# Performance work log

Hardware: AMD Instinct MI355X
Metric: run time of the kernel (lower is better)

Reference implementation:

```python
import jax, jax.numpy as jnp
from jax import lax
import numpy as np

B, T, F, H, L = 256, 512, 16, 256, 2


def _lstm_layer(x, w_ih, w_hh, b_ih, b_hh):
    # x: [B, T, in]; w_ih: [4H, in]; w_hh: [4H, H]; biases: [4H]
    # PyTorch gate order: i, f, g, o
    x_proj = jnp.einsum('bti,gi->btg', x, w_ih) + b_ih + b_hh  # [B, T, 4H]
    h0 = jnp.zeros((x.shape[0], w_hh.shape[1]), x.dtype)
    c0 = h0

    def step(carry, xp):
        h, c = carry
        gates = xp + h @ w_hh.T  # [B, 4H]
        i, f, g, o = jnp.split(gates, 4, axis=-1)
        c = jax.nn.sigmoid(f) * c + jax.nn.sigmoid(i) * jnp.tanh(g)
        h = jax.nn.sigmoid(o) * jnp.tanh(c)
        return (h, c), h

    _, hs = lax.scan(step, (h0, c0), jnp.swapaxes(x_proj, 0, 1))  # [T, B, H]
    return jnp.swapaxes(hs, 0, 1)  # [B, T, H]


def setup_inputs() -> dict:
    key = jax.random.key(0)
    ks = jax.random.split(key, 16)
    x = jax.random.normal(ks[0], (B, T, F), dtype=jnp.float32)
    lengths = jax.random.randint(ks[1], (B,), 1, T + 1)  # in [1, T]
    s = 1.0 / np.sqrt(H)
    u = lambda k, shape: jax.random.uniform(k, shape, jnp.float32, -s, s)
    inp = {'x': x, 'lengths': lengths}
    in_dims = [F, H]
    for l in range(L):
        inp[f'w_ih{l}'] = u(ks[2 + 4 * l], (4 * H, in_dims[l]))
        inp[f'w_hh{l}'] = u(ks[3 + 4 * l], (4 * H, H))
        inp[f'b_ih{l}'] = u(ks[4 + 4 * l], (4 * H,))
        inp[f'b_hh{l}'] = u(ks[5 + 4 * l], (4 * H,))
    inp['fc_w'] = u(ks[10], (1, H))
    inp['fc_b'] = u(ks[11], (1,))
    return inp


def reference(x, lengths, w_ih0, w_hh0, b_ih0, b_hh0,
              w_ih1, w_hh1, b_ih1, b_hh1, fc_w, fc_b):
    # Packed LSTM: outputs at t >= length never influence last_outputs
    # (recurrence only flows forward in time), so running the dense
    # full-length LSTM and gathering at lengths-1 is mathematically identical.
    h = _lstm_layer(x, w_ih0, w_hh0, b_ih0, b_hh0)
    h = _lstm_layer(h, w_ih1, w_hh1, b_ih1, b_hh1)
    last = h[jnp.arange(h.shape[0]), lengths - 1]  # [B, H]
    return jax.nn.relu(last) @ fc_w.T + fc_b  # [B, 1]
```

## Files before the change

kernel.cpp:

```cpp
#include <hip/hip_runtime.h>
#include <hip/hip_fp16.h>


#define Tc 32
#define NCHUNK 16

#define OFF_IH0   0
#define OFF_B0    16384
#define OFF_B1    17408
#define OFF_C0S   18432
#define OFF_C1S   84480
#define OFF_H1S   150528
#define OFF_HLAST 216576
#define FP_END    282624
#define H_HH0  0
#define H_HH1  262144
#define H_IH1  524288
#define H_H0C  786432
#define H0SLOT 2113536
#define H_XP1  5013504
#define XPSLOT 8454144

#define SMEM_BYTES 85184

typedef _Float16 v2h __attribute__((ext_vector_type(2)));

__device__ __forceinline__ unsigned packh2(float a, float b) {
  __half2 h = __floats2half2_rn(a, b);
  return *(unsigned*)&h;
}
__device__ __forceinline__ float4 dot4(const float4 w, const v2h h, float4 acc) {
  const v2h* wg = (const v2h*)&w;
  acc.x = __builtin_amdgcn_fdot2(wg[0], h, acc.x, false);
  acc.y = __builtin_amdgcn_fdot2(wg[1], h, acc.y, false);
  acc.z = __builtin_amdgcn_fdot2(wg[2], h, acc.z, false);
  acc.w = __builtin_amdgcn_fdot2(wg[3], h, acc.w, false);
  return acc;
}
__device__ __forceinline__ float sigf(float x) {
  return __fdividef(1.f, 1.f + __expf(-x));
}
__device__ __forceinline__ float tanhf_fast(float x) {
  float ax = fabsf(x);
  float e = __expf(-2.f * ax);
  float t = __fdividef(1.f - e, 1.f + e);
  return copysignf(t, x);
}
__device__ __forceinline__ float h2f(unsigned short s) {
  __half h = __builtin_bit_cast(__half, s);
  return __half2float(h);
}
__device__ __forceinline__ float4 cvt4(ushort4 v) {
  float4 r;
  r.x = h2f(v.x); r.y = h2f(v.y); r.z = h2f(v.z); r.w = h2f(v.w);
  return r;
}
__device__ __forceinline__ v2h u2h(unsigned v) {
  return __builtin_bit_cast(v2h, v);
}
__device__ __forceinline__ float4 f4add(float4 a, float4 b) {
  a.x += b.x; a.y += b.y; a.z += b.z; a.w += b.w;
  return a;
}

__global__ __launch_bounds__(256) void prep_kernel(
    const float* __restrict__ w_ih0, const float* __restrict__ w_hh0,
    const float* __restrict__ b_ih0, const float* __restrict__ b_hh0,
    const float* __restrict__ w_ih1, const float* __restrict__ w_hh1,
    const float* __restrict__ b_ih1, const float* __restrict__ b_hh1,
    float* __restrict__ ws) {
  const int idx = blockIdx.x * blockDim.x + threadIdx.x;
  const int g = idx & 3, u = (idx >> 2) & 255, p = idx >> 10;
  const int j = g * 256 + u;
  unsigned* h16u = (unsigned*)(ws + FP_END);
  h16u[H_HH0 / 2 + idx] = packh2(w_hh0[j * 256 + 2 * p], w_hh0[j * 256 + 2 * p + 1]);
  h16u[H_HH1 / 2 + idx] = packh2(w_hh1[j * 256 + 2 * p], w_hh1[j * 256 + 2 * p + 1]);
  h16u[H_IH1 / 2 + idx] = packh2(w_ih1[j * 256 + 2 * p], w_ih1[j * 256 + 2 * p + 1]);
  if (idx < 8192) {
    ((unsigned*)(ws + OFF_IH0))[idx] =
        packh2(w_ih0[j * 16 + 2 * p], w_ih0[j * 16 + 2 * p + 1]);
  }
  if (idx < 1024) {
    ws[OFF_B0 + idx] = b_ih0[j] + b_hh0[j];
    ws[OFF_B1 + idx] = b_ih1[j] + b_hh1[j];
  }
}

__global__ __launch_bounds__(1024) void fused_kernel(
    float* __restrict__ ws, const float* __restrict__ x,
    const int* __restrict__ lengths, int step) {
  extern __shared__ __align__(16) char smem_raw[];
  const int bid = blockIdx.x;
  const int tid = threadIdx.x;
  __half* h16 = (__half*)(ws + FP_END);
  unsigned short* h0cS = (unsigned short*)(h16 + H_H0C);
  unsigned short* xpS = (unsigned short*)(h16 + H_XP1);

  if (bid < 86) {
    if (step >= NCHUNK) return;
    const int kc = step;
    const int kq = tid >> 8, u = tid & 255;
    const int bg = bid * 3;
    unsigned short* hb = (unsigned short*)smem_raw;
    unsigned* xsp = (unsigned*)(smem_raw + 3072);
    float4* sc4 = (float4*)(smem_raw + 3264);
    float4* wxl = (float4*)(smem_raw + 52416);

    int len[3];
    #pragma unroll
    for (int b = 0; b < 3; ++b) len[b] = (bg + b < 256) ? lengths[bg + b] : 1;
    const int tmaxb = max(len[0], max(len[1], len[2]));
    if (kc * Tc >= tmaxb) return;
    const int tend = min(Tc, tmaxb - kc * Tc);
    const int slot = kc & 1, slotP = slot ^ 1;

    {
      const float4* gwx = (const float4*)(ws + OFF_IH0);
      wxl[tid] = gwx[tid];
      wxl[tid + 1024] = gwx[tid + 1024];
    }

    const float4* wq = (const float4*)(h16 + H_HH0) + (size_t)(kq * 32) * 256 + u;
    const float4 bias = ((const float4*)(ws + OFF_B0))[u];

    float cc = 0.f;
    if (kq < 3) {
      unsigned short hv = 0;
      if (kc > 0) {
        hv = h0cS[(size_t)slotP * H0SLOT + ((size_t)(bg + kq) * 32 + 31) * 256 + u];
        cc = ws[OFF_C0S + (bg + kq) * 256 + u];
      }
      hb[0 * 768 + kq * 256 + u] = hv;
    }
    if (tid < 24) {
      int b = tid >> 3, i = tid & 7;
      int bb = min(bg + b, 255);
      const float* xp = x + (size_t)bb * 8192 + (kc * Tc) * 16;
      xsp[0 * 24 + b * 8 + i] = packh2(xp[2 * i], xp[2 * i + 1]);
    }
    __syncthreads();

    for (int tc = 0; tc < tend; ++tc) {
      const int cur = tc & 1, nxt = cur ^ 1;
      float4 A0, A1, A2;
      if (kq == 3) {
        A0 = bias; A1 = bias; A2 = bias;
        #pragma unroll
        for (int p = 0; p < 8; ++p) {
          float4 w = wxl[p * 256 + u];
          A0 = dot4(w, u2h(xsp[cur * 24 + 0 * 8 + p]), A0);
          A1 = dot4(w, u2h(xsp[cur * 24 + 1 * 8 + p]), A1);
          A2 = dot4(w, u2h(xsp[cur * 24 + 2 * 8 + p]), A2);
        }
      } else {
        A0 = make_float4(0, 0, 0, 0); A1 = A0; A2 = A0;
      }

      {
        const float4* h0r0 = (const float4*)(hb + cur * 768 + 0 * 256 + kq * 64);
        const float4* h0r1 = (const float4*)(hb + cur * 768 + 1 * 256 + kq * 64);
        const float4* h0r2 = (const float4*)(hb + cur * 768 + 2 * 256 + kq * 64);
        float4 B[3][4];
        #pragma unroll
        for (int p = 0; p < 4; ++p) {
          B[0][p] = wq[p * 256];
          B[1][p] = wq[(4 + p) * 256];
        }
        #pragma unroll
        for (int g = 0; g < 8; ++g) {
          if (g + 2 < 8) {
            #pragma unroll
            for (int p = 0; p < 4; ++p)
              B[(g + 2) % 3][p] = wq[((g + 2) * 4 + p) * 256];
          }
          const float4* wbuf = B[g % 3];
          float4 h40 = h0r0[g], h41 = h0r1[g], h42 = h0r2[g];
          const v2h* hp0 = (const v2h*)&h40;
          const v2h* hp1 = (const v2h*)&h41;
          const v2h* hp2 = (const v2h*)&h42;
          #pragma unroll
          for (int q = 0; q < 4; ++q) {
            A0 = dot4(wbuf[q], hp0[q], A0);
            A1 = dot4(wbuf[q], hp1[q], A1);
            A2 = dot4(wbuf[q], hp2[q], A2);
          }
        }
      }

      sc4[(kq * 3 + 0) * 256 + u] = A0;
      sc4[(kq * 3 + 1) * 256 + u] = A1;
      sc4[(kq * 3 + 2) * 256 + u] = A2;
      __syncthreads();

      if (kq < 3) {
        float4 A = f4add(f4add(sc4[(0 * 3 + kq) * 256 + u],
                               sc4[(1 * 3 + kq) * 256 + u]),
                         f4add(sc4[(2 * 3 + kq) * 256 + u],
                               sc4[(3 * 3 + kq) * 256 + u]));
        float ig = sigf(A.x), fg = sigf(A.y);
        float gg = tanhf_fast(A.z), og = sigf(A.w);
        cc = fg * cc + ig * gg;
        float h = og * tanhf_fast(cc);
        unsigned short hu = __half_as_ushort(__float2half(h));
        hb[nxt * 768 + kq * 256 + u] = hu;
        h0cS[(size_t)slot * H0SLOT + ((size_t)(bg + kq) * 32 + tc) * 256 + u] = hu;
      } else if (tid >= 768 && tid < 792) {
        int bi = tid - 768, b = bi >> 3, i = bi & 7;
        int bb = min(bg + b, 255);
        int tn = min(kc * Tc + tc + 1, 511);
        const float* xp = x + (size_t)bb * 8192 + tn * 16;
        xsp[nxt * 24 + b * 8 + i] = packh2(xp[2 * i], xp[2 * i + 1]);
      }
      __syncthreads();
    }
    if (kq < 3) ws[OFF_C0S + (bg + kq) * 256 + u] = cc;

  } else if (bid < 172) {
    if (step < 2 || step >= NCHUNK + 2) return;
    const int kc = step - 2;
    const int kq = tid >> 8, u = tid & 255;
    const int bg = (bid - 86) * 3;
    unsigned short* h1b = (unsigned short*)smem_raw;
    float4* sc4 = (float4*)(smem_raw + 3072);

    int len[3];
    #pragma unroll
    for (int b = 0; b < 3; ++b) len[b] = (bg + b < 256) ? lengths[bg + b] : 1;
    const int tmaxb = max(len[0], max(len[1], len[2]));
    if (kc * Tc >= tmaxb) return;
    const int tend = min(Tc, tmaxb - kc * Tc);
    const int slot = kc & 1;

    const float4* wq = (const float4*)(h16 + H_HH1) + (size_t)(kq * 32) * 256 + u;

    float cc = 0.f, hout = 0.f;
    int lenb = 1;
    const unsigned short* xb = xpS;
    ushort4 xc;
    if (kq < 3) {
      lenb = len[kq];
      float hv = 0.f;
      if (kc > 0) {
        hv = ws[OFF_H1S + (bg + kq) * 256 + u];
        cc = ws[OFF_C1S + (bg + kq) * 256 + u];
      }
      h1b[0 * 768 + kq * 256 + u] = __half_as_ushort(__float2half(hv));
      xb = xpS + (size_t)slot * XPSLOT + (size_t)(bg + kq) * 32768 + u * 4;
      xc = *(const ushort4*)(xb);
    }
    __syncthreads();

    for (int tc = 0; tc < tend; ++tc) {
      const int cur = tc & 1, nxt = cur ^ 1;
      float4 A0 = make_float4(0, 0, 0, 0), A1 = A0, A2 = A0;

      {
        const float4* r0 = (const float4*)(h1b + cur * 768 + 0 * 256 + kq * 64);
        const float4* r1 = (const float4*)(h1b + cur * 768 + 1 * 256 + kq * 64);
        const float4* r2 = (const float4*)(h1b + cur * 768 + 2 * 256 + kq * 64);
        float4 B[3][4];
        #pragma unroll
        for (int p = 0; p < 4; ++p) {
          B[0][p] = wq[p * 256];
          B[1][p] = wq[(4 + p) * 256];
        }
        #pragma unroll
        for (int g = 0; g < 8; ++g) {
          if (g + 2 < 8) {
            #pragma unroll
            for (int p = 0; p < 4; ++p)
              B[(g + 2) % 3][p] = wq[((g + 2) * 4 + p) * 256];
          }
          const float4* wbuf = B[g % 3];
          float4 h40 = r0[g], h41 = r1[g], h42 = r2[g];
          const v2h* hp0 = (const v2h*)&h40;
          const v2h* hp1 = (const v2h*)&h41;
          const v2h* hp2 = (const v2h*)&h42;
          #pragma unroll
          for (int q = 0; q < 4; ++q) {
            A0 = dot4(wbuf[q], hp0[q], A0);
            A1 = dot4(wbuf[q], hp1[q], A1);
            A2 = dot4(wbuf[q], hp2[q], A2);
          }
        }
      }

      sc4[(kq * 3 + 0) * 256 + u] = A0;
      sc4[(kq * 3 + 1) * 256 + u] = A1;
      sc4[(kq * 3 + 2) * 256 + u] = A2;
      __syncthreads();

      if (kq < 3) {
        ushort4 xn;
        if (tc + 1 < tend) xn = *(const ushort4*)(xb + (tc + 1) * 1024);
        float4 A = f4add(f4add(sc4[(0 * 3 + kq) * 256 + u],
                               sc4[(1 * 3 + kq) * 256 + u]),
                         f4add(sc4[(2 * 3 + kq) * 256 + u],
                               sc4[(3 * 3 + kq) * 256 + u]));
        A = f4add(A, cvt4(xc));
        float ig = sigf(A.x), fg = sigf(A.y);
        float gg = tanhf_fast(A.z), og = sigf(A.w);
        cc = fg * cc + ig * gg;
        float h = og * tanhf_fast(cc);
        hout = h;
        h1b[nxt * 768 + kq * 256 + u] = __half_as_ushort(__float2half(h));
        const int t = kc * Tc + tc;
        if (t == lenb - 1) ws[OFF_HLAST + (bg + kq) * 256 + u] = h;
        xc = xn;
      }
      __syncthreads();
    }
    if (kq < 3) {
      ws[OFF_C1S + (bg + kq) * 256 + u] = cc;
      ws[OFF_H1S + (bg + kq) * 256 + u] = hout;
    }

  } else {
    if (step < 1 || step >= NCHUNK + 1) return;
    if (bid >= 236) return;
    const int kc = step - 1;
    const int gid = bid - 172;
    const int b0g = gid * 4;
    const int rp = tid >> 9;
    const int rt = tid & 63, wv = (tid >> 6) & 7;
    __half2* hc2 = (__half2*)smem_raw;

    int lmax = 0;
    #pragma unroll
    for (int i = 0; i < 4; ++i) lmax = max(lmax, lengths[b0g + i]);
    if (kc * Tc >= lmax) return;
    const int slot = kc & 1;

    {
      const unsigned short* src =
          h0cS + (size_t)slot * H0SLOT + (size_t)b0g * 8192;
      const int cl = tid & 127, pg = tid >> 7;
      #pragma unroll
      for (int pp = 0; pp < 16; pp += 4) {
        const int p0 = pg * 16 + pp;
        uint4 v = *(const uint4*)(src + (size_t)cl * 256 + p0 * 2);
        unsigned* d = (unsigned*)hc2;
        d[(p0 + 0) * 128 + cl] = v.x;
        d[(p0 + 1) * 128 + cl] = v.y;
        d[(p0 + 2) * 128 + cl] = v.z;
        d[(p0 + 3) * 128 + cl] = v.w;
      }
    }
    __syncthreads();

    const __half* Wb = h16 + H_IH1;
    unsigned short* xdst = xpS + (size_t)slot * XPSLOT;
    #pragma unroll 1
    for (int cp = 0; cp < 2; ++cp) {
      const int uA = rp * 128 + rt, uB = uA + 64;
      const int c0 = cp * 64 + wv * 8;
      const float4 bA = ((const float4*)(ws + OFF_B1))[uA];
      const float4 bB = ((const float4*)(ws + OFF_B1))[uB];
      float accA[4][8], accB[4][8];
      #pragma unroll
      for (int g = 0; g < 4; ++g)
        #pragma unroll
        for (int cc = 0; cc < 8; ++cc) {
          accA[g][cc] = ((const float*)&bA)[g];
          accB[g][cc] = ((const float*)&bB)[g];
        }
      #pragma unroll 2
      for (int p = 0; p < 128; ++p) {
        float4 wA = *(const float4*)(Wb + (size_t)p * 2048 + uA * 8);
        float4 wB = *(const float4*)(Wb + (size_t)p * 2048 + uB * 8);
        float4 h0v = *(const float4*)(hc2 + p * 128 + c0);
        float4 h1v = *(const float4*)(hc2 + p * 128 + c0 + 4);
        const v2h* ga = (const v2h*)&wA;
        const v2h* gb = (const v2h*)&wB;
        const v2h* hv = (const v2h*)&h0v;
        const v2h* hw = (const v2h*)&h1v;
        #pragma unroll
        for (int g = 0; g < 4; ++g) {
          #pragma unroll
          for (int cc = 0; cc < 4; ++cc) {
            accA[g][cc] = __builtin_amdgcn_fdot2(ga[g], hv[cc], accA[g][cc], false);
            accA[g][cc + 4] = __builtin_amdgcn_fdot2(ga[g], hw[cc], accA[g][cc + 4], false);
            accB[g][cc] = __builtin_amdgcn_fdot2(gb[g], hv[cc], accB[g][cc], false);
            accB[g][cc + 4] = __builtin_amdgcn_fdot2(gb[g], hw[cc], accB[g][cc + 4], false);
          }
        }
      }
      #pragma unroll
      for (int cc = 0; cc < 8; ++cc) {
        const int col = c0 + cc;
        const size_t cb = ((size_t)(b0g + (col >> 5)) * 32 + (col & 31)) * 1024;
        ushort4 oA, oB;
        oA.x = __half_as_ushort(__float2half(accA[0][cc]));
        oA.y = __half_as_ushort(__float2half(accA[1][cc]));
        oA.z = __half_as_ushort(__float2half(accA[2][cc]));
        oA.w = __half_as_ushort(__float2half(accA[3][cc]));
        oB.x = __half_as_ushort(__float2half(accB[0][cc]));
        oB.y = __half_as_ushort(__float2half(accB[1][cc]));
        oB.z = __half_as_ushort(__float2half(accB[2][cc]));
        oB.w = __half_as_ushort(__float2half(accB[3][cc]));
        *(ushort4*)(xdst + cb + uA * 4) = oA;
        *(ushort4*)(xdst + cb + uB * 4) = oB;
      }
    }
  }
}

__global__ __launch_bounds__(256) void fc_kernel(
    const float* __restrict__ ws, const float* __restrict__ fc_w,
    const float* __restrict__ fc_b, float* __restrict__ out) {
  __shared__ float red[256];
  const int tid = threadIdx.x;
  const int b = blockIdx.x;
  red[tid] = fmaxf(ws[OFF_HLAST + b * 256 + tid], 0.f) * fc_w[tid];
  __syncthreads();
  #pragma unroll
  for (int s = 128; s > 0; s >>= 1) {
    if (tid < s) red[tid] += red[tid + s];
    __syncthreads();
  }
  if (tid == 0) out[b] = red[0] + fc_b[0];
}

extern "C" void kernel_launch(void* const* d_in, const int* in_sizes, int n_in,
                              void* d_out, int out_size, void* d_ws, size_t ws_size,
                              hipStream_t stream) {
  const float* x     = (const float*)d_in[0];
  const int*   lens  = (const int*)d_in[1];
  const float* w_ih0 = (const float*)d_in[2];
  const float* w_hh0 = (const float*)d_in[3];
  const float* b_ih0 = (const float*)d_in[4];
  const float* b_hh0 = (const float*)d_in[5];
  const float* w_ih1 = (const float*)d_in[6];
  const float* w_hh1 = (const float*)d_in[7];
  const float* b_ih1 = (const float*)d_in[8];
  const float* b_hh1 = (const float*)d_in[9];
  const float* fc_w  = (const float*)d_in[10];
  const float* fc_b  = (const float*)d_in[11];
  float* out = (float*)d_out;
  float* ws  = (float*)d_ws;

  hipLaunchKernelGGL(prep_kernel, dim3(512), dim3(256), 0, stream,
                     w_ih0, w_hh0, b_ih0, b_hh0, w_ih1, w_hh1, b_ih1, b_hh1, ws);
  hipFuncSetAttribute(reinterpret_cast<const void*>(fused_kernel),
                      hipFuncAttributeMaxDynamicSharedMemorySize, SMEM_BYTES);
  for (int k = 0; k < NCHUNK + 2; ++k) {
    hipLaunchKernelGGL(fused_kernel, dim3(236), dim3(1024), SMEM_BYTES, stream,
                       ws, x, lens, k);
  }
  hipLaunchKernelGGL(fc_kernel, dim3(256), dim3(256), 0, stream,
                     ws, fc_w, fc_b, out);
}
```

Before: 3.338 ms.

## Use MFMA 16x16x32 for LSTM recurrences with 16-sequence blocks

Replaces the fdot2-based recurrent matvec, which processed 3 sequences per block with a cross-wave shared-memory reduction, by MFMA f16 16x16x32 tiles. Each block now handles 16 batch rows, and each wave owns 16 hidden units across all 4 gates. Weights are repacked into MFMA fragment layout, and the layer-1 input projection output is re-laid out to match the accumulator fragments. This drops the per-step partial-sum reduction and its extra barrier, and cuts the recurrent blocks from 172 to 32. In exchange, much less of the GPU is occupied during the serial recurrence, and per-block serial length grows with the longest sequence in each group of 16.

```diff
diff --git a/kernel.cpp b/kernel.cpp
--- a/kernel.cpp
+++ b/kernel.cpp
@@ -21,21 +21,14 @@
 #define H_XP1  5013504
 #define XPSLOT 8454144
 
-#define SMEM_BYTES 85184
-
-typedef _Float16 v2h __attribute__((ext_vector_type(2)));
+#define SMEM_BYTES 32768
+
+typedef _Float16 v8h __attribute__((ext_vector_type(8)));
+typedef float v4f __attribute__((ext_vector_type(4)));
 
 __device__ __forceinline__ unsigned packh2(float a, float b) {
   __half2 h = __floats2half2_rn(a, b);
   return *(unsigned*)&h;
-}
-__device__ __forceinline__ float4 dot4(const float4 w, const v2h h, float4 acc) {
-  const v2h* wg = (const v2h*)&w;
-  acc.x = __builtin_amdgcn_fdot2(wg[0], h, acc.x, false);
-  acc.y = __builtin_amdgcn_fdot2(wg[1], h, acc.y, false);
-  acc.z = __builtin_amdgcn_fdot2(wg[2], h, acc.z, false);
-  acc.w = __builtin_amdgcn_fdot2(wg[3], h, acc.w, false);
-  return acc;
 }
 __device__ __forceinline__ float sigf(float x) {
   return __fdividef(1.f, 1.f + __expf(-x));
@@ -50,18 +43,13 @@
   __half h = __builtin_bit_cast(__half, s);
   return __half2float(h);
 }
-__device__ __forceinline__ float4 cvt4(ushort4 v) {
-  float4 r;
-  r.x = h2f(v.x); r.y = h2f(v.y); r.z = h2f(v.z); r.w = h2f(v.w);
-  return r;
-}
-__device__ __forceinline__ v2h u2h(unsigned v) {
-  return __builtin_bit_cast(v2h, v);
-}
-__device__ __forceinline__ float4 f4add(float4 a, float4 b) {
-  a.x += b.x; a.y += b.y; a.z += b.z; a.w += b.w;
-  return a;
-}
+__device__ __forceinline__ float h_at(uint4 v, int i) {
+  unsigned wd = ((const unsigned*)&v)[i >> 1];
+  unsigned short s = (i & 1) ? (unsigned short)(wd >> 16) : (unsigned short)wd;
+  return h2f(s);
+}
+
+typedef _Float16 v2h __attribute__((ext_vector_type(2)));
 
 __global__ __launch_bounds__(256) void prep_kernel(
     const float* __restrict__ w_ih0, const float* __restrict__ w_hh0,
@@ -70,17 +58,35 @@
     const float* __restrict__ b_ih1, const float* __restrict__ b_hh1,
     float* __restrict__ ws) {
   const int idx = blockIdx.x * blockDim.x + threadIdx.x;
-  const int g = idx & 3, u = (idx >> 2) & 255, p = idx >> 10;
-  const int j = g * 256 + u;
   unsigned* h16u = (unsigned*)(ws + FP_END);
-  h16u[H_HH0 / 2 + idx] = packh2(w_hh0[j * 256 + 2 * p], w_hh0[j * 256 + 2 * p + 1]);
-  h16u[H_HH1 / 2 + idx] = packh2(w_hh1[j * 256 + 2 * p], w_hh1[j * 256 + 2 * p + 1]);
-  h16u[H_IH1 / 2 + idx] = packh2(w_ih1[j * 256 + 2 * p], w_ih1[j * 256 + 2 * p + 1]);
-  if (idx < 8192) {
-    ((unsigned*)(ws + OFF_IH0))[idx] =
-        packh2(w_ih0[j * 16 + 2 * p], w_ih0[j * 16 + 2 * p + 1]);
+  {
+    const int q2 = idx * 2;
+    const int j = q2 & 7, l = (q2 >> 3) & 63, ks = (q2 >> 9) & 7;
+    const int U = (q2 >> 12) & 15, g = q2 >> 16;
+    const int row = g * 256 + U * 16 + (l & 15);
+    const int k0 = ks * 32 + ((l >> 4) & 3) * 8 + j;
+    h16u[H_HH0 / 2 + idx] =
+        packh2(w_hh0[row * 256 + k0], w_hh0[row * 256 + k0 + 1]);
+    h16u[H_HH1 / 2 + idx] =
+        packh2(w_hh1[row * 256 + k0], w_hh1[row * 256 + k0 + 1]);
+  }
+  {
+    const int g = idx & 3, u = (idx >> 2) & 255, p = idx >> 10;
+    const int j = g * 256 + u;
+    h16u[H_IH1 / 2 + idx] =
+        packh2(w_ih1[j * 256 + 2 * p], w_ih1[j * 256 + 2 * p + 1]);
+  }
+  if (idx < 16384) {
+    const int q2 = idx * 2;
+    const int j = q2 & 7, l = (q2 >> 3) & 63, U = (q2 >> 9) & 15, g = q2 >> 13;
+    const int row = g * 256 + U * 16 + (l & 15);
+    const int k0 = (l >> 4) * 8 + j;
+    float a = (k0 < 16) ? w_ih0[row * 16 + k0] : 0.f;
+    float b = (k0 + 1 < 16) ? w_ih0[row * 16 + k0 + 1] : 0.f;
+    ((unsigned*)(ws + OFF_IH0))[idx] = packh2(a, b);
   }
   if (idx < 1024) {
+    const int j = (idx & 3) * 256 + (idx >> 2);
     ws[OFF_B0 + idx] = b_ih0[j] + b_hh0[j];
     ws[OFF_B1 + idx] = b_ih1[j] + b_hh1[j];
   }
@@ -96,311 +102,262 @@
   unsigned short* h0cS = (unsigned short*)(h16 + H_H0C);
   unsigned short* xpS = (unsigned short*)(h16 + H_XP1);
 
-  if (bid < 86) {
-    if (step >= NCHUNK) return;
-    const int kc = step;
-    const int kq = tid >> 8, u = tid & 255;
-    const int bg = bid * 3;
-    unsigned short* hb = (unsigned short*)smem_raw;
-    unsigned* xsp = (unsigned*)(smem_raw + 3072);
-    float4* sc4 = (float4*)(smem_raw + 3264);
-    float4* wxl = (float4*)(smem_raw + 52416);
-
-    int len[3];
-    #pragma unroll
-    for (int b = 0; b < 3; ++b) len[b] = (bg + b < 256) ? lengths[bg + b] : 1;
-    const int tmaxb = max(len[0], max(len[1], len[2]));
+  if (bid < 32) {
+    const bool isL0 = (bid < 16);
+    int kc;
+    if (isL0) { if (step >= NCHUNK) return; kc = step; }
+    else { if (step < 2 || step >= NCHUNK + 2) return; kc = step - 2; }
+    const int G = isL0 ? bid : (bid - 16);
+    const int bg = G * 16;
+    const int w = tid >> 6, l = tid & 63;
+    const int n = l & 15, m0 = (l >> 4) * 4;
+    const int u = w * 16 + n;
+    unsigned short* hf = (unsigned short*)smem_raw;
+    unsigned short* xf = hf + 8192;
+
+    int tmaxb = 1;
+    for (int i = 0; i < 16; ++i) tmaxb = max(tmaxb, lengths[bg + i]);
     if (kc * Tc >= tmaxb) return;
     const int tend = min(Tc, tmaxb - kc * Tc);
     const int slot = kc & 1, slotP = slot ^ 1;
 
-    {
-      const float4* gwx = (const float4*)(ws + OFF_IH0);
-      wxl[tid] = gwx[tid];
-      wxl[tid + 1024] = gwx[tid + 1024];
-    }
-
-    const float4* wq = (const float4*)(h16 + H_HH0) + (size_t)(kq * 32) * 256 + u;
-    const float4 bias = ((const float4*)(ws + OFF_B0))[u];
-
-    float cc = 0.f;
-    if (kq < 3) {
+    const float4* WB =
+        (const float4*)(h16 + (isL0 ? H_HH0 : H_HH1));
+    const int ksp = u >> 5, lp0 = ((u >> 3) & 3) * 16, jh = u & 7;
+
+    float bias[4];
+    v8h bx[4];
+    if (isL0) {
+      const float4* WX = (const float4*)(ws + OFF_IH0);
+      #pragma unroll
+      for (int g = 0; g < 4; ++g) {
+        bx[g] = __builtin_bit_cast(v8h, WX[(g * 16 + w) * 64 + l]);
+        bias[g] = ws[OFF_B0 + u * 4 + g];
+      }
+    }
+    int len4[4];
+    #pragma unroll
+    for (int r = 0; r < 4; ++r) len4[r] = lengths[bg + m0 + r];
+
+    float c4[4] = {0.f, 0.f, 0.f, 0.f};
+    float h4[4] = {0.f, 0.f, 0.f, 0.f};
+    #pragma unroll
+    for (int r = 0; r < 4; ++r) {
       unsigned short hv = 0;
       if (kc > 0) {
-        hv = h0cS[(size_t)slotP * H0SLOT + ((size_t)(bg + kq) * 32 + 31) * 256 + u];
-        cc = ws[OFF_C0S + (bg + kq) * 256 + u];
-      }
-      hb[0 * 768 + kq * 256 + u] = hv;
-    }
-    if (tid < 24) {
-      int b = tid >> 3, i = tid & 7;
-      int bb = min(bg + b, 255);
-      const float* xp = x + (size_t)bb * 8192 + (kc * Tc) * 16;
-      xsp[0 * 24 + b * 8 + i] = packh2(xp[2 * i], xp[2 * i + 1]);
-    }
+        if (isL0) {
+          hv = h0cS[(size_t)slotP * H0SLOT +
+                    ((size_t)(bg + m0 + r) * 32 + 31) * 256 + u];
+          c4[r] = ws[OFF_C0S + (bg + m0 + r) * 256 + u];
+        } else {
+          hv = __half_as_ushort(
+              __float2half(ws[OFF_H1S + (bg + m0 + r) * 256 + u]));
+          c4[r] = ws[OFF_C1S + (bg + m0 + r) * 256 + u];
+        }
+      }
+      hf[(ksp * 64 + lp0 + m0 + r) * 8 + jh] = hv;
+    }
+    const unsigned short* xpb = nullptr;
+    uint4 q0, q1;
+    if (isL0) {
+      if (w == 0) {
+        if (l >= 32) {
+          uint4 z = {0, 0, 0, 0};
+          *(uint4*)(xf + l * 8) = z;
+          *(uint4*)(xf + (64 + l) * 8) = z;
+        } else {
+          const float* xp =
+              x + (size_t)(bg + (l & 15)) * 8192 + (kc * Tc) * 16 + (l >> 4) * 8;
+          float4 a = *(const float4*)xp, b = *(const float4*)(xp + 4);
+          uint4 v = {packh2(a.x, a.y), packh2(a.z, a.w), packh2(b.x, b.y),
+                     packh2(b.z, b.w)};
+          *(uint4*)(xf + l * 8) = v;
+        }
+      }
+    } else {
+      xpb = xpS + (size_t)slot * XPSLOT + (size_t)G * 524288 + u * 64 + m0 * 4;
+      q0 = *(const uint4*)(xpb);
+      q1 = *(const uint4*)(xpb + 8);
+    }
+    v8h bf[4], bn[4];
+    #pragma unroll
+    for (int g = 0; g < 4; ++g)
+      bf[g] = __builtin_bit_cast(v8h, WB[((g * 16 + w) * 8 + 0) * 64 + l]);
     __syncthreads();
 
     for (int tc = 0; tc < tend; ++tc) {
       const int cur = tc & 1, nxt = cur ^ 1;
-      float4 A0, A1, A2;
-      if (kq == 3) {
-        A0 = bias; A1 = bias; A2 = bias;
-        #pragma unroll
-        for (int p = 0; p < 8; ++p) {
-          float4 w = wxl[p * 256 + u];
-          A0 = dot4(w, u2h(xsp[cur * 24 + 0 * 8 + p]), A0);
-          A1 = dot4(w, u2h(xsp[cur * 24 + 1 * 8 + p]), A1);
-          A2 = dot4(w, u2h(xsp[cur * 24 + 2 * 8 + p]), A2);
-        }
+      v4f A[4];
+      uint4 p0n, p1n;
+      if (isL0) {
+        #pragma unroll
+        for (int g = 0; g < 4; ++g) {
+          v4f bz = {bias[g], bias[g], bias[g], bias[g]};
+          A[g] = bz;
+        }
+        v8h ax = __builtin_bit_cast(v8h, *(const float4*)(xf + (cur * 64 + l) * 8));
+        #pragma unroll
+        for (int g = 0; g < 4; ++g)
+          A[g] = __builtin_amdgcn_mfma_f32_16x16x32_f16(ax, bx[g], A[g], 0, 0, 0);
       } else {
-        A0 = make_float4(0, 0, 0, 0); A1 = A0; A2 = A0;
-      }
-
-      {
-        const float4* h0r0 = (const float4*)(hb + cur * 768 + 0 * 256 + kq * 64);
-        const float4* h0r1 = (const float4*)(hb + cur * 768 + 1 * 256 + kq * 64);
-        const float4* h0r2 = (const float4*)(hb + cur * 768 + 2 * 256 + kq * 64);
-        float4 B[3][4];
-        #pragma unroll
-        for (int p = 0; p < 4; ++p) {
-          B[0][p] = wq[p * 256];
-          B[1][p] = wq[(4 + p) * 256];
-        }
-        #pragma unroll
-        for (int g = 0; g < 8; ++g) {
-          if (g + 2 < 8) {
-            #pragma unroll
-            for (int p = 0; p < 4; ++p)
-              B[(g + 2) % 3][p] = wq[((g + 2) * 4 + p) * 256];
-          }
-          const float4* wbuf = B[g % 3];
-          float4 h40 = h0r0[g], h41 = h0r1[g], h42 = h0r2[g];
-          const v2h* hp0 = (const v2h*)&h40;
-          const v2h* hp1 = (const v2h*)&h41;
-          const v2h* hp2 = (const v2h*)&h42;
+        if (tc + 1 < tend) {
+          p0n = *(const uint4*)(xpb + (size_t)(tc + 1) * 16384);
+          p1n = *(const uint4*)(xpb + (size_t)(tc + 1) * 16384 + 8);
+        }
+        #pragma unroll
+        for (int g = 0; g < 4; ++g) {
+          v4f av;
+          av[0] = h_at(q0, g);
+          av[1] = h_at(q0, 4 + g);
+          av[2] = h_at(q1, g);
+          av[3] = h_at(q1, 4 + g);
+          A[g] = av;
+        }
+      }
+      #pragma unroll
+      for (int ks = 0; ks < 8; ++ks) {
+        if (ks < 7) {
           #pragma unroll
-          for (int q = 0; q < 4; ++q) {
-            A0 = dot4(wbuf[q], hp0[q], A0);
-            A1 = dot4(wbuf[q], hp1[q], A1);
-            A2 = dot4(wbuf[q], hp2[q], A2);
-          }
-        }
-      }
-
-      sc4[(kq * 3 + 0) * 256 + u] = A0;
-      sc4[(kq * 3 + 1) * 256 + u] = A1;
-      sc4[(kq * 3 + 2) * 256 + u] = A2;
+          for (int g = 0; g < 4; ++g)
+            bn[g] = __builtin_bit_cast(
+                v8h, WB[((g * 16 + w) * 8 + ks + 1) * 64 + l]);
+        }
+        v8h ah = __builtin_bit_cast(
+            v8h, *(const float4*)(hf + ((cur * 8 + ks) * 64 + l) * 8));
+        #pragma unroll
+        for (int g = 0; g < 4; ++g)
+          A[g] = __builtin_amdgcn_mfma_f32_16x16x32_f16(ah, bf[g], A[g], 0, 0, 0);
+        #pragma unroll
+        for (int g = 0; g < 4; ++g) bf[g] = bn[g];
+      }
+      #pragma unroll
+      for (int r = 0; r < 4; ++r) {
+        float ig = sigf(A[0][r]), fg = sigf(A[1][r]);
+        float gg = tanhf_fast(A[2][r]), og = sigf(A[3][r]);
+        c4[r] = fg * c4[r] + ig * gg;
+        h4[r] = og * tanhf_fast(c4[r]);
+        unsigned short hv = __half_as_ushort(__float2half(h4[r]));
+        hf[((nxt * 8 + ksp) * 64 + lp0 + m0 + r) * 8 + jh] = hv;
+        if (isL0) {
+          h0cS[(size_t)slot * H0SLOT +
+               ((size_t)(bg + m0 + r) * 32 + tc) * 256 + u] = hv;
+        } else {
+          if (kc * Tc + tc == len4[r] - 1)
+            ws[OFF_HLAST + (bg + m0 + r) * 256 + u] = h4[r];
+        }
+      }
+      if (isL0) {
+        if (w == 0 && l < 32) {
+          int tn = min(kc * Tc + tc + 1, 511);
+          const float* xp =
+              x + (size_t)(bg + (l & 15)) * 8192 + tn * 16 + (l >> 4) * 8;
+          float4 a = *(const float4*)xp, b = *(const float4*)(xp + 4);
+          uint4 v = {packh2(a.x, a.y), packh2(a.z, a.w), packh2(b.x, b.y),
+                     packh2(b.z, b.w)};
+          *(uint4*)(xf + (nxt * 64 + l) * 8) = v;
+        }
+      } else {
+        q0 = p0n;
+        q1 = p1n;
+      }
+      #pragma unroll
+      for (int g = 0; g < 4; ++g)
+        bf[g] = __builtin_bit_cast(v8h, WB[((g * 16 + w) * 8 + 0) * 64 + l]);
       __syncthreads();
-
-      if (kq < 3) {
-        float4 A = f4add(f4add(sc4[(0 * 3 + kq) * 256 + u],
-                               sc4[(1 * 3 + kq) * 256 + u]),
-                         f4add(sc4[(2 * 3 + kq) * 256 + u],
-                               sc4[(3 * 3 + kq) * 256 + u]));
-        float ig = sigf(A.x), fg = sigf(A.y);
-        float gg = tanhf_fast(A.z), og = sigf(A.w);
-        cc = fg * cc + ig * gg;
-        float h = og * tanhf_fast(cc);
-        unsigned short hu = __half_as_ushort(__float2half(h));
-        hb[nxt * 768 + kq * 256 + u] = hu;
-        h0cS[(size_t)slot * H0SLOT + ((size_t)(bg + kq) * 32 + tc) * 256 + u] = hu;
-      } else if (tid >= 768 && tid < 792) {
-        int bi = tid - 768, b = bi >> 3, i = bi & 7;
-        int bb = min(bg + b, 255);
-        int tn = min(kc * Tc + tc + 1, 511);
-        const float* xp = x + (size_t)bb * 8192 + tn * 16;
-        xsp[nxt * 24 + b * 8 + i] = packh2(xp[2 * i], xp[2 * i + 1]);
-      }
-      __syncthreads();
-    }
-    if (kq < 3) ws[OFF_C0S + (bg + kq) * 256 + u] = cc;
-
-  } else if (bid < 172) {
-    if (step < 2 || step >= NCHUNK + 2) return;
-    const int kc = step - 2;
-    const int kq = tid >> 8, u = tid & 255;
-    const int bg = (bid - 86) * 3;
-    unsigned short* h1b = (unsigned short*)smem_raw;
-    float4* sc4 = (float4*)(smem_raw + 3072);
-
-    int len[3];
-    #pragma unroll
-    for (int b = 0; b < 3; ++b) len[b] = (bg + b < 256) ? lengths[bg + b] : 1;
-    const int tmaxb = max(len[0], max(len[1], len[2]));
-    if (kc * Tc >= tmaxb) return;
-    const int tend = min(Tc, tmaxb - kc * Tc);
-    const int slot = kc & 1;
-
-    const float4* wq = (const float4*)(h16 + H_HH1) + (size_t)(kq * 32) * 256 + u;
-
-    float cc = 0.f, hout = 0.f;
-    int lenb = 1;
-    const unsigned short* xb = xpS;
-    ushort4 xc;
-    if (kq < 3) {
-      lenb = len[kq];
-      float hv = 0.f;
-      if (kc > 0) {
-        hv = ws[OFF_H1S + (bg + kq) * 256 + u];
-        cc = ws[OFF_C1S + (bg + kq) * 256 + u];
-      }
-      h1b[0 * 768 + kq * 256 + u] = __half_as_ushort(__float2half(hv));
-      xb = xpS + (size_t)slot * XPSLOT + (size_t)(bg + kq) * 32768 + u * 4;
-      xc = *(const ushort4*)(xb);
-    }
-    __syncthreads();
-
-    for (int tc = 0; tc < tend; ++tc) {
-      const int cur = tc & 1, nxt = cur ^ 1;
-      float4 A0 = make_float4(0, 0, 0, 0), A1 = A0, A2 = A0;
-
-      {
-        const float4* r0 = (const float4*)(h1b + cur * 768 + 0 * 256 + kq * 64);
-        const float4* r1 = (const float4*)(h1b + cur * 768 + 1 * 256 + kq * 64);
-        const float4* r2 = (const float4*)(h1b + cur * 768 + 2 * 256 + kq * 64);
-        float4 B[3][4];
-        #pragma unroll
-        for (int p = 0; p < 4; ++p) {
-          B[0][p] = wq[p * 256];
-          B[1][p] = wq[(4 + p) * 256];
-        }
-        #pragma unroll
-        for (int g = 0; g < 8; ++g) {
-          if (g + 2 < 8) {
-            #pragma unroll
-            for (int p = 0; p < 4; ++p)
-              B[(g + 2) % 3][p] = wq[((g + 2) * 4 + p) * 256];
-          }
-          const float4* wbuf = B[g % 3];
-          float4 h40 = r0[g], h41 = r1[g], h42 = r2[g];
-          const v2h* hp0 = (const v2h*)&h40;
-          const v2h* hp1 = (const v2h*)&h41;
-          const v2h* hp2 = (const v2h*)&h42;
-          #pragma unroll
-          for (int q = 0; q < 4; ++q) {
-            A0 = dot4(wbuf[q], hp0[q], A0);
-            A1 = dot4(wbuf[q], hp1[q], A1);
-            A2 = dot4(wbuf[q], hp2[q], A2);
-          }
-        }
-      }
-
-      sc4[(kq * 3 + 0) * 256 + u] = A0;
-      sc4[(kq * 3 + 1) * 256 + u] = A1;
-      sc4[(kq * 3 + 2) * 256 + u] = A2;
-      __syncthreads();
-
-      if (kq < 3) {
-        ushort4 xn;
-        if (tc + 1 < tend) xn = *(const ushort4*)(xb + (tc + 1) * 1024);
-        float4 A = f4add(f4add(sc4[(0 * 3 + kq) * 256 + u],
-                               sc4[(1 * 3 + kq) * 256 + u]),
-                         f4add(sc4[(2 * 3 + kq) * 256 + u],
-                               sc4[(3 * 3 + kq) * 256 + u]));
-        A = f4add(A, cvt4(xc));
-        float ig = sigf(A.x), fg = sigf(A.y);
-        float gg = tanhf_fast(A.z), og = sigf(A.w);
-        cc = fg * cc + ig * gg;
-        float h = og * tanhf_fast(cc);
-        hout = h;
-        h1b[nxt * 768 + kq * 256 + u] = __half_as_ushort(__float2half(h));
-        const int t = kc * Tc + tc;
-        if (t == lenb - 1) ws[OFF_HLAST + (bg + kq) * 256 + u] = h;
-        xc = xn;
-      }
-      __syncthreads();
-    }
-    if (kq < 3) {
-      ws[OFF_C1S + (bg + kq) * 256 + u] = cc;
-      ws[OFF_H1S + (bg + kq) * 256 + u] = hout;
+    }
+    #pragma unroll
+    for (int r = 0; r < 4; ++r) {
+      if (isL0) {
+        ws[OFF_C0S + (bg + m0 + r) * 256 + u] = c4[r];
+      } else {
+        ws[OFF_C1S + (bg + m0 + r) * 256 + u] = c4[r];
+        ws[OFF_H1S + (bg + m0 + r) * 256 + u] = h4[r];
+      }
     }
 
   } else {
     if (step < 1 || step >= NCHUNK + 1) return;
-    if (bid >= 236) return;
+    if (bid >= 160) return;
     const int kc = step - 1;
-    const int gid = bid - 172;
-    const int b0g = gid * 4;
-    const int rp = tid >> 9;
-    const int rt = tid & 63, wv = (tid >> 6) & 7;
+    const int gid = bid - 32;
+    const int bg2 = gid * 2;
+    const int G = bg2 >> 4, mb = bg2 & 15;
     __half2* hc2 = (__half2*)smem_raw;
 
-    int lmax = 0;
-    #pragma unroll
-    for (int i = 0; i < 4; ++i) lmax = max(lmax, lengths[b0g + i]);
+    int lmax = max(lengths[bg2], lengths[bg2 + 1]);
     if (kc * Tc >= lmax) return;
     const int slot = kc & 1;
 
     {
       const unsigned short* src =
-          h0cS + (size_t)slot * H0SLOT + (size_t)b0g * 8192;
-      const int cl = tid & 127, pg = tid >> 7;
-      #pragma unroll
-      for (int pp = 0; pp < 16; pp += 4) {
-        const int p0 = pg * 16 + pp;
+          h0cS + (size_t)slot * H0SLOT + (size_t)bg2 * 8192;
+      const int cl = tid & 63, pg = tid >> 6;
+      #pragma unroll
+      for (int pp = 0; pp < 8; pp += 4) {
+        const int p0 = pg * 8 + pp;
         uint4 v = *(const uint4*)(src + (size_t)cl * 256 + p0 * 2);
         unsigned* d = (unsigned*)hc2;
-        d[(p0 + 0) * 128 + cl] = v.x;
-        d[(p0 + 1) * 128 + cl] = v.y;
-        d[(p0 + 2) * 128 + cl] = v.z;
-        d[(p0 + 3) * 128 + cl] = v.w;
+        d[(p0 + 0) * 64 + cl] = v.x;
+        d[(p0 + 1) * 64 + cl] = v.y;
+        d[(p0 + 2) * 64 + cl] = v.z;
+        d[(p0 + 3) * 64 + cl] = v.w;
       }
     }
     __syncthreads();
 
     const __half* Wb = h16 + H_IH1;
-    unsigned short* xdst = xpS + (size_t)slot * XPSLOT;
-    #pragma unroll 1
-    for (int cp = 0; cp < 2; ++cp) {
-      const int uA = rp * 128 + rt, uB = uA + 64;
-      const int c0 = cp * 64 + wv * 8;
-      const float4 bA = ((const float4*)(ws + OFF_B1))[uA];
-      const float4 bB = ((const float4*)(ws + OFF_B1))[uB];
-      float accA[4][8], accB[4][8];
-      #pragma unroll
-      for (int g = 0; g < 4; ++g)
-        #pragma unroll
-        for (int cc = 0; cc < 8; ++cc) {
-          accA[g][cc] = ((const float*)&bA)[g];
-          accB[g][cc] = ((const float*)&bB)[g];
-        }
-      #pragma unroll 2
-      for (int p = 0; p < 128; ++p) {
-        float4 wA = *(const float4*)(Wb + (size_t)p * 2048 + uA * 8);
-        float4 wB = *(const float4*)(Wb + (size_t)p * 2048 + uB * 8);
-        float4 h0v = *(const float4*)(hc2 + p * 128 + c0);
-        float4 h1v = *(const float4*)(hc2 + p * 128 + c0 + 4);
-        const v2h* ga = (const v2h*)&wA;
-        const v2h* gb = (const v2h*)&wB;
-        const v2h* hv = (const v2h*)&h0v;
-        const v2h* hw = (const v2h*)&h1v;
-        #pragma unroll
-        for (int g = 0; g < 4; ++g) {
-          #pragma unroll
-          for (int cc = 0; cc < 4; ++cc) {
-            accA[g][cc] = __builtin_amdgcn_fdot2(ga[g], hv[cc], accA[g][cc], false);
-            accA[g][cc + 4] = __builtin_amdgcn_fdot2(ga[g], hw[cc], accA[g][cc + 4], false);
-            accB[g][cc] = __builtin_amdgcn_fdot2(gb[g], hv[cc], accB[g][cc], false);
-            accB[g][cc + 4] = __builtin_amdgcn_fdot2(gb[g], hw[cc], accB[g][cc + 4], false);
-          }
-        }
-      }
+    unsigned short* xdst =
+        xpS + (size_t)slot * XPSLOT + (size_t)G * 524288;
+    const int rp = tid >> 9, rt = tid & 63, wv = (tid >> 6) & 7;
+    const int uA = rp * 128 + rt, uB = uA + 64;
+    const int c0 = wv * 8;
+    const float4 bA = ((const float4*)(ws + OFF_B1))[uA];
+    const float4 bB = ((const float4*)(ws + OFF_B1))[uB];
+    float accA[4][8], accB[4][8];
+    #pragma unroll
+    for (int g = 0; g < 4; ++g)
       #pragma unroll
       for (int cc = 0; cc < 8; ++cc) {
-        const int col = c0 + cc;
-        const size_t cb = ((size_t)(b0g + (col >> 5)) * 32 + (col & 31)) * 1024;
-        ushort4 oA, oB;
-        oA.x = __half_as_ushort(__float2half(accA[0][cc]));
-        oA.y = __half_as_ushort(__float2half(accA[1][cc]));
-        oA.z = __half_as_ushort(__float2half(accA[2][cc]));
-        oA.w = __half_as_ushort(__float2half(accA[3][cc]));
-        oB.x = __half_as_ushort(__float2half(accB[0][cc]));
-        oB.y = __half_as_ushort(__float2half(accB[1][cc]));
-        oB.z = __half_as_ushort(__float2half(accB[2][cc]));
-        oB.w = __half_as_ushort(__float2half(accB[3][cc]));
-        *(ushort4*)(xdst + cb + uA * 4) = oA;
-        *(ushort4*)(xdst + cb + uB * 4) = oB;
-      }
+        accA[g][cc] = ((const float*)&bA)[g];
+        accB[g][cc] = ((const float*)&bB)[g];
+      }
+    #pragma unroll 2
+    for (int p = 0; p < 128; ++p) {
+      float4 wA = *(const float4*)(Wb + (size_t)p * 2048 + uA * 8);
+      float4 wB = *(const float4*)(Wb + (size_t)p * 2048 + uB * 8);
+      float4 h0v = *(const float4*)(hc2 + p * 64 + c0);
+      float4 h1v = *(const float4*)(hc2 + p * 64 + c0 + 4);
+      const v2h* ga = (const v2h*)&wA;
+      const v2h* gb = (const v2h*)&wB;
+      const v2h* hv = (const v2h*)&h0v;
+      const v2h* hw = (const v2h*)&h1v;
+      #pragma unroll
+      for (int g = 0; g < 4; ++g) {
+        #pragma unroll
+        for (int cc = 0; cc < 4; ++cc) {
+          accA[g][cc] = __builtin_amdgcn_fdot2(ga[g], hv[cc], accA[g][cc], false);
+          accA[g][cc + 4] = __builtin_amdgcn_fdot2(ga[g], hw[cc], accA[g][cc + 4], false);
+          accB[g][cc] = __builtin_amdgcn_fdot2(gb[g], hv[cc], accB[g][cc], false);
+          accB[g][cc + 4] = __builtin_amdgcn_fdot2(gb[g], hw[cc], accB[g][cc + 4], false);
+        }
+      }
+    }
+    #pragma unroll
+    for (int cc = 0; cc < 8; ++cc) {
+      const int col = c0 + cc;
+      const int t = col & 31, m = mb + (col >> 5);
+      const size_t base = ((size_t)t * 256) * 64 + (size_t)m * 4;
+      ushort4 oA, oB;
+      oA.x = __half_as_ushort(__float2half(accA[0][cc]));
+      oA.y = __half_as_ushort(__float2half(accA[1][cc]));
+      oA.z = __half_as_ushort(__float2half(accA[2][cc]));
+      oA.w = __half_as_ushort(__float2half(accA[3][cc]));
+      oB.x = __half_as_ushort(__float2half(accB[0][cc]));
+      oB.y = __half_as_ushort(__float2half(accB[1][cc]));
+      oB.z = __half_as_ushort(__float2half(accB[2][cc]));
+      oB.w = __half_as_ushort(__float2half(accB[3][cc]));
+      *(ushort4*)(xdst + base + (size_t)uA * 64) = oA;
+      *(ushort4*)(xdst + base + (size_t)uB * 64) = oB;
     }
   }
 }
@@ -444,7 +401,7 @@
   hipFuncSetAttribute(reinterpret_cast<const void*>(fused_kernel),
                       hipFuncAttributeMaxDynamicSharedMemorySize, SMEM_BYTES);
   for (int k = 0; k < NCHUNK + 2; ++k) {
-    hipLaunchKernelGGL(fused_kernel, dim3(236), dim3(1024), SMEM_BYTES, stream,
+    hipLaunchKernelGGL(fused_kernel, dim3(160), dim3(1024), SMEM_BYTES, stream,
                        ws, x, lens, k);
   }
   hipLaunchKernelGGL(fc_kernel, dim3(256), dim3(256), 0, stream,
```

Result: slower. 5.792 ms (+73.5%).
